# Performance work log

Hardware: AMD Instinct MI355X
Metric: run time of the kernel (lower is better)

The kernel has to match this reference:

```python
import jax, jax.numpy as jnp
import numpy as np

N_TOKENS = 8192
TOP_K = 2
N_EXPERTS = 8
D_IN = 2048
D_OUT = 2048


def setup_inputs() -> dict:
    key = jax.random.key(0)
    k1, k2, k3, k4 = jax.random.split(key, 4)
    inputs = jax.random.normal(k1, (N_TOKENS, D_IN), dtype=jnp.float32)
    # stored as [E, out, in], matching nn.Parameter(torch.empty(E, output_size, input_size))
    expert_weights = 0.02 * jax.random.normal(k2, (N_EXPERTS, D_OUT, D_IN), dtype=jnp.float32)
    gates = jax.nn.softmax(jax.random.normal(k3, (N_TOKENS, TOP_K), dtype=jnp.float32), axis=-1)
    # per (token, slot) expert assignment, then sort by expert as the router would
    flat_experts = jax.random.randint(k4, (N_TOKENS * TOP_K,), 0, N_EXPERTS, dtype=jnp.int32)
    sorted_scattered_idxs = jnp.argsort(flat_experts).astype(jnp.int32)
    sorted_expert_idxs = flat_experts[sorted_scattered_idxs]
    expert_offsets = jnp.cumsum(jnp.bincount(flat_experts, length=N_EXPERTS)).astype(jnp.int32)
    return {
        "inputs": inputs,
        "expert_weights": expert_weights,
        "gates": gates,
        "k": TOP_K,
        "sorted_expert_idxs": sorted_expert_idxs,
        "sorted_scattered_idxs": sorted_scattered_idxs,
        "expert_offsets": expert_offsets,
    }


def reference(inputs, expert_weights, gates, k, sorted_expert_idxs, sorted_scattered_idxs, expert_offsets):
    N, d_in = inputs.shape
    E = expert_weights.shape[0]
    Nk = N * k
    # forward permutes weight [E, out, in] -> [E, in, out]
    W = jnp.transpose(expert_weights, (0, 2, 1))
    d_out = W.shape[-1]
    # invert the sort: expert id for each flat (token, slot) index
    expert_per_flat = jnp.zeros((Nk,), dtype=sorted_expert_idxs.dtype).at[
        sorted_scattered_idxs].set(sorted_expert_idxs)
    # scatter2scatter: out_flat[j] = x[j // k] @ W[expert_per_flat[j]]
    x_rep = jnp.repeat(inputs, k, axis=0)  # [N*k, d_in]
    out_flat = jnp.zeros((Nk, d_out), dtype=inputs.dtype)
    for e in range(E):  # small fixed expert count; masked grouped GEMM
        mask = (expert_per_flat == e)[:, None]
        out_flat = out_flat + jnp.where(mask, x_rep, 0.0) @ W[e]
    # combine: (gates.unsqueeze(1) @ output_expanded).squeeze(1)
    out = jnp.einsum('nk,nkd->nd', gates, out_flat.reshape(N, k, d_out))
    return out
```

## Files before the change

### kernel.cpp

```cpp
#include <hip/hip_runtime.h>
#include <hip/hip_bf16.h>
#include <stdint.h>

#define NTOK   8192
#define TOPK   2
#define NEXP   8
#define DIN    2048
#define DOUT   2048
#define NK     (NTOK*TOPK)

#define BM 256
#define BN 128
#define BK 32
#define KTILES  (DIN/BK)
#define SLOT    24576
#define NBUF    3

typedef __bf16 bf16_8 __attribute__((ext_vector_type(8)));
typedef float  f32x4  __attribute__((ext_vector_type(4)));

__device__ __forceinline__ void gl2lds16(const void* g, void* l) {
  auto gp = reinterpret_cast<const __attribute__((address_space(1))) uint32_t*>(
      reinterpret_cast<uintptr_t>(g));
  auto lp = reinterpret_cast<__attribute__((address_space(3))) uint32_t*>(
      reinterpret_cast<uintptr_t>(l));
  __builtin_amdgcn_global_load_lds(gp, lp, 16, 0, 0);
}

__global__ void cvt_all(const float4* __restrict__ w, uint4* __restrict__ wD,
                        const float4* __restrict__ x, uint4* __restrict__ xD,
                        int nW) {
  int b = blockIdx.x;
  const float4* src;
  uint4* dst;
  int i;
  if (b < nW) { src = w; dst = wD; i = b * 256 + threadIdx.x; }
  else        { src = x; dst = xD; i = (b - nW) * 256 + threadIdx.x; }
  float4 a0 = src[2 * i];
  float4 a1 = src[2 * i + 1];
  union { __bf16 h[8]; uint4 u; } r;
  r.h[0] = (__bf16)a0.x; r.h[1] = (__bf16)a0.y; r.h[2] = (__bf16)a0.z; r.h[3] = (__bf16)a0.w;
  r.h[4] = (__bf16)a1.x; r.h[5] = (__bf16)a1.y; r.h[6] = (__bf16)a1.z; r.h[7] = (__bf16)a1.w;
  dst[i] = r.u;
}

__global__ __launch_bounds__(512, 4)
void moe_gemm(const __bf16* __restrict__ X,
              const __bf16* __restrict__ W,
              const int* __restrict__ ssi,
              const int* __restrict__ offs,
              __bf16* __restrict__ flat)
{
  __shared__ char lds[NBUF * SLOT];
  __shared__ int  sTok[BM];
  __shared__ int  sF[BM];

  const int tid = threadIdx.x;
  const int nwg = gridDim.x;
  const int b0  = blockIdx.x;
  const int bid = (b0 & 7) * (nwg >> 3) + (b0 >> 3);
  const int nt  = bid & 15;
  const int mtg = bid >> 4;

  int start = 0, end = 0, e, cum = 0, prev = 0, mloc = 0, found = 0;
  for (e = 0; e < NEXP; ++e) {
    int oe  = offs[e];
    int seg = oe - prev;
    int t   = (seg + BM - 1) >> 8;
    if (mtg < cum + t) { start = prev; end = oe; mloc = mtg - cum; found = 1; break; }
    cum += t; prev = oe;
  }
  if (!found) return;

  const int m0 = start + mloc * BM;

  if (tid < BM) {
    int p     = m0 + tid;
    int valid = p < end;
    int f     = ssi[valid ? p : (end - 1)];
    sTok[tid] = f >> 1;
    sF[tid]   = valid ? f : -1;
  }
  __syncthreads();

  const int rs = tid >> 2;
  const int kc = (tid & 3) ^ ((tid >> 3) & 3);
  const __bf16* pA0 = X + (size_t)sTok[rs]       * DIN + kc * 8;
  const __bf16* pA1 = X + (size_t)sTok[rs + 128] * DIN + kc * 8;
  const __bf16* wBp = W + (size_t)e * DOUT * DIN + (size_t)(nt * BN) * DIN;
  const __bf16* pB0 = wBp + (size_t)rs * DIN + kc * 8;
  char* wsl = (char*)lds + (tid >> 6) * 1024;

  gl2lds16(pA0, wsl);           gl2lds16(pA1, wsl + 8192);
  gl2lds16(pB0, wsl + 16384);
  pA0 += BK; pA1 += BK; pB0 += BK;
  gl2lds16(pA0, wsl + SLOT);    gl2lds16(pA1, wsl + SLOT + 8192);
  gl2lds16(pB0, wsl + SLOT + 16384);
  pA0 += BK; pA1 += BK; pB0 += BK;

  const int w   = tid >> 6;
  const int l   = tid & 63;
  const int wm  = w >> 1, wn = w & 1;
  const int lr  = l & 15;
  const int kq  = l >> 4;
  const int kqs = kq ^ ((lr >> 1) & 3);
  const char* aBase = (const char*)lds + (wm * 64 + lr) * 64 + kqs * 16;
  const char* bBase = (const char*)lds + 16384 + (wn * 64 + lr) * 64 + kqs * 16;

  asm volatile("s_waitcnt vmcnt(3)" ::: "memory");
  __builtin_amdgcn_s_barrier();

  f32x4 acc[4][4] = {};
  int rOff = 0;
  int sOff = 2 * SLOT;

  for (int t = 0; t < KTILES; ++t) {
    if (t < KTILES - 2) {
      char* d = wsl + sOff;
      gl2lds16(pA0, d);  gl2lds16(pA1, d + 8192);  gl2lds16(pB0, d + 16384);
      pA0 += BK; pA1 += BK; pB0 += BK;
      sOff = (sOff == (NBUF - 1) * SLOT) ? 0 : sOff + SLOT;
    }

    const char* aB = aBase + rOff;
    const char* bB = bBase + rOff;
    rOff = (rOff == (NBUF - 1) * SLOT) ? 0 : rOff + SLOT;

    bf16_8 af[4], bf[4];
#pragma unroll
    for (int i = 0; i < 4; ++i) af[i] = *(const bf16_8*)(aB + i * 1024);
#pragma unroll
    for (int i = 0; i < 4; ++i) bf[i] = *(const bf16_8*)(bB + i * 1024);

#pragma unroll
    for (int am = 0; am < 4; ++am)
#pragma unroll
      for (int bn = 0; bn < 4; ++bn)
        acc[am][bn] = __builtin_amdgcn_mfma_f32_16x16x32_bf16(
            af[am], bf[bn], acc[am][bn], 0, 0, 0);

    if (t < KTILES - 2)       { asm volatile("s_waitcnt vmcnt(3)" ::: "memory"); }
    else if (t == KTILES - 2) { asm volatile("s_waitcnt vmcnt(0)" ::: "memory"); }
    if (t < KTILES - 1) __builtin_amdgcn_s_barrier();
  }

  const int colBase = nt * BN + wn * 64 + lr;
  const int rq = kq * 4;
#pragma unroll
  for (int am = 0; am < 4; ++am) {
#pragma unroll
    for (int v = 0; v < 4; ++v) {
      int rl = wm * 64 + am * 16 + rq + v;
      int f  = sF[rl];
      if (f < 0) continue;
      __bf16* row = flat + (size_t)f * DOUT + colBase;
#pragma unroll
      for (int bn = 0; bn < 4; ++bn)
        row[bn * 16] = (__bf16)acc[am][bn][v];
    }
  }
}

__global__ __launch_bounds__(256)
void combine(const __bf16* __restrict__ flat, const float* __restrict__ gates,
             float* __restrict__ out) {
  const int n = blockIdx.x;
  const int c = threadIdx.x * 8;
  bf16_8 y0 = *(const bf16_8*)(flat + (size_t)(2 * n)     * DOUT + c);
  bf16_8 y1 = *(const bf16_8*)(flat + (size_t)(2 * n + 1) * DOUT + c);
  const float2 g = *(const float2*)(gates + 2 * n);
  float o[8];
#pragma unroll
  for (int j = 0; j < 8; ++j)
    o[j] = g.x * (float)y0[j] + g.y * (float)y1[j];
  float4* dst = (float4*)(out + (size_t)n * DOUT + c);
  dst[0] = *(float4*)&o[0];
  dst[1] = *(float4*)&o[4];
}

extern "C" void kernel_launch(void* const* d_in, const int* in_sizes, int n_in,
                              void* d_out, int out_size, void* d_ws, size_t ws_size,
                              hipStream_t stream) {
  const float* inputs = (const float*)d_in[0];
  const float* ew     = (const float*)d_in[1];
  const float* gates  = (const float*)d_in[2];
  const int*   ssi    = (const int*)d_in[5];
  const int*   offs   = (const int*)d_in[6];
  float* out = (float*)d_out;

  __bf16* wsW = (__bf16*)d_ws;
  __bf16* wsX = wsW + (size_t)NEXP * DOUT * DIN;
  __bf16* wsF = wsX + (size_t)NTOK * DIN;

  const int n8w = NEXP * DOUT * DIN / 8;
  const int n8x = NTOK * DIN / 8;
  const int nWb = n8w / 256, nXb = n8x / 256;
  cvt_all<<<nWb + nXb, 256, 0, stream>>>((const float4*)ew, (uint4*)wsW,
                                         (const float4*)inputs, (uint4*)wsX, nWb);

  moe_gemm<<<72 * 16, 512, 0, stream>>>(wsX, wsW, ssi, offs, wsF);
  combine<<<NTOK, 256, 0, stream>>>(wsF, gates, out);
}
```

Measured before the change: 434.7 us.

## Split A/B LDS buffers with deeper A prefetch and drop index staging

Separates the LDS ring into four buffers for the gathered A tile and two for the contiguous B weight tile. Gathered token rows are prefetched three tiles ahead while weights stay double-buffered. The shared-memory staging of token and flat indices, with its extra barrier, is removed, and indices are read straight from global memory both in the prologue and in the epilogue. LDS grows from 72 KB to 80 KB, which could reduce occupancy, and the epilogue now issues scattered global index loads.

New measurement: 438.1 us. No clear change (+0.8%).

```diff
diff --git a/kernel.cpp b/kernel.cpp
--- a/kernel.cpp
+++ b/kernel.cpp
@@ -13,8 +13,11 @@
 #define BN 128
 #define BK 32
 #define KTILES  (DIN/BK)
-#define SLOT    24576
-#define NBUF    3
+#define ASLOT   16384
+#define BSLOT   8192
+#define NBUFA   4
+#define NBUFB   2
+#define BOFF    (NBUFA*ASLOT)
 
 typedef __bf16 bf16_8 __attribute__((ext_vector_type(8)));
 typedef float  f32x4  __attribute__((ext_vector_type(4)));
@@ -51,9 +54,7 @@
               const int* __restrict__ offs,
               __bf16* __restrict__ flat)
 {
-  __shared__ char lds[NBUF * SLOT];
-  __shared__ int  sTok[BM];
-  __shared__ int  sF[BM];
+  __shared__ char lds[NBUFA * ASLOT + NBUFB * BSLOT];
 
   const int tid = threadIdx.x;
   const int nwg = gridDim.x;
@@ -74,29 +75,25 @@
 
   const int m0 = start + mloc * BM;
 
-  if (tid < BM) {
-    int p     = m0 + tid;
-    int valid = p < end;
-    int f     = ssi[valid ? p : (end - 1)];
-    sTok[tid] = f >> 1;
-    sF[tid]   = valid ? f : -1;
-  }
-  __syncthreads();
-
   const int rs = tid >> 2;
   const int kc = (tid & 3) ^ ((tid >> 3) & 3);
-  const __bf16* pA0 = X + (size_t)sTok[rs]       * DIN + kc * 8;
-  const __bf16* pA1 = X + (size_t)sTok[rs + 128] * DIN + kc * 8;
+  int p0 = m0 + rs, p1 = m0 + rs + 128;
+  int tok0 = ssi[p0 < end ? p0 : (end - 1)] >> 1;
+  int tok1 = ssi[p1 < end ? p1 : (end - 1)] >> 1;
+  const __bf16* pA0 = X + (size_t)tok0 * DIN + kc * 8;
+  const __bf16* pA1 = X + (size_t)tok1 * DIN + kc * 8;
   const __bf16* wBp = W + (size_t)e * DOUT * DIN + (size_t)(nt * BN) * DIN;
   const __bf16* pB0 = wBp + (size_t)rs * DIN + kc * 8;
   char* wsl = (char*)lds + (tid >> 6) * 1024;
 
-  gl2lds16(pA0, wsl);           gl2lds16(pA1, wsl + 8192);
-  gl2lds16(pB0, wsl + 16384);
-  pA0 += BK; pA1 += BK; pB0 += BK;
-  gl2lds16(pA0, wsl + SLOT);    gl2lds16(pA1, wsl + SLOT + 8192);
-  gl2lds16(pB0, wsl + SLOT + 16384);
-  pA0 += BK; pA1 += BK; pB0 += BK;
+  gl2lds16(pB0, wsl + BOFF);
+  pB0 += BK;
+  gl2lds16(pA0, wsl);              gl2lds16(pA1, wsl + 8192);
+  pA0 += BK; pA1 += BK;
+  gl2lds16(pA0, wsl + ASLOT);      gl2lds16(pA1, wsl + ASLOT + 8192);
+  pA0 += BK; pA1 += BK;
+  gl2lds16(pA0, wsl + 2 * ASLOT);  gl2lds16(pA1, wsl + 2 * ASLOT + 8192);
+  pA0 += BK; pA1 += BK;
 
   const int w   = tid >> 6;
   const int l   = tid & 63;
@@ -105,26 +102,26 @@
   const int kq  = l >> 4;
   const int kqs = kq ^ ((lr >> 1) & 3);
   const char* aBase = (const char*)lds + (wm * 64 + lr) * 64 + kqs * 16;
-  const char* bBase = (const char*)lds + 16384 + (wn * 64 + lr) * 64 + kqs * 16;
-
-  asm volatile("s_waitcnt vmcnt(3)" ::: "memory");
+  const char* bBase = (const char*)lds + BOFF + (wn * 64 + lr) * 64 + kqs * 16;
+
+  asm volatile("s_waitcnt vmcnt(4)" ::: "memory");
   __builtin_amdgcn_s_barrier();
 
   f32x4 acc[4][4] = {};
-  int rOff = 0;
-  int sOff = 2 * SLOT;
 
   for (int t = 0; t < KTILES; ++t) {
-    if (t < KTILES - 2) {
-      char* d = wsl + sOff;
-      gl2lds16(pA0, d);  gl2lds16(pA1, d + 8192);  gl2lds16(pB0, d + 16384);
-      pA0 += BK; pA1 += BK; pB0 += BK;
-      sOff = (sOff == (NBUF - 1) * SLOT) ? 0 : sOff + SLOT;
+    if (t < KTILES - 1) {
+      gl2lds16(pB0, wsl + BOFF + (((t + 1) & 1) << 13));
+      pB0 += BK;
     }
-
-    const char* aB = aBase + rOff;
-    const char* bB = bBase + rOff;
-    rOff = (rOff == (NBUF - 1) * SLOT) ? 0 : rOff + SLOT;
+    if (t < KTILES - 3) {
+      char* d = wsl + (((t + 3) & 3) << 14);
+      gl2lds16(pA0, d);  gl2lds16(pA1, d + 8192);
+      pA0 += BK; pA1 += BK;
+    }
+
+    const char* aB = aBase + ((t & 3) << 14);
+    const char* bB = bBase + ((t & 1) << 13);
 
     bf16_8 af[4], bf[4];
 #pragma unroll
@@ -139,8 +136,8 @@
         acc[am][bn] = __builtin_amdgcn_mfma_f32_16x16x32_bf16(
             af[am], bf[bn], acc[am][bn], 0, 0, 0);
 
-    if (t < KTILES - 2)       { asm volatile("s_waitcnt vmcnt(3)" ::: "memory"); }
-    else if (t == KTILES - 2) { asm volatile("s_waitcnt vmcnt(0)" ::: "memory"); }
+    if (t < KTILES - 3)       { asm volatile("s_waitcnt vmcnt(2)" ::: "memory"); }
+    else if (t < KTILES - 1)  { asm volatile("s_waitcnt vmcnt(0)" ::: "memory"); }
     if (t < KTILES - 1) __builtin_amdgcn_s_barrier();
   }
 
@@ -151,8 +148,9 @@
 #pragma unroll
     for (int v = 0; v < 4; ++v) {
       int rl = wm * 64 + am * 16 + rq + v;
-      int f  = sF[rl];
-      if (f < 0) continue;
+      int p  = m0 + rl;
+      if (p >= end) continue;
+      int f = ssi[p];
       __bf16* row = flat + (size_t)f * DOUT + colBase;
 #pragma unroll
       for (int bn = 0; bn < 4; ++bn)
```
